# Performance work log

Measured on AMD Instinct MI355X. Metric: run time of the kernel, lower is better.

## Reference

```python
import jax, jax.numpy as jnp
from jax import lax
import numpy as np

CIN, COUT, K, STYLE_DIM = 256, 256, 3, 512
N_LAYERS = 4
TYPES = ("same", "upsample", "same", "downsample")
SCALE = 1.0 / float(np.sqrt(CIN * K ** 2))  # source uses kernel_size**2 even in 1D
EPS = 1e-8
_BK = np.array([1.0, 3.0, 3.0, 1.0], dtype=np.float32)
BLUR_K = _BK / _BK.sum()  # normalized FIR kernel, len 4


def _blur(x, kern, pad):
    # x: (B, C, L); depthwise FIR correlation after zero-padding (upfirdn1d, up=down=1)
    B, C, _ = x.shape
    xp = jnp.pad(x, ((0, 0), (0, 0), (pad[0], pad[1])))
    w = jnp.broadcast_to(kern.astype(x.dtype)[None, None, :], (C, 1, kern.shape[0]))
    return lax.conv_general_dilated(xp, w, (1,), 'VALID', feature_group_count=C,
                                    dimension_numbers=('NCH', 'OIH', 'NCH'))


def _conv_same(x, w):
    # x: (Cin, L), w: (Cout, Cin, K); padding = (K-1)//2, stride 1
    p = (K - 1) // 2
    return lax.conv_general_dilated(x[None], w, (1,), [(p, p)],
                                    dimension_numbers=('NCH', 'OIH', 'NCH'))[0]


def _conv_down(x, w):
    # stride-2 valid conv (padding handled by preceding blur)
    return lax.conv_general_dilated(x[None], w, (2,), 'VALID',
                                    dimension_numbers=('NCH', 'OIH', 'NCH'))[0]


def _conv_up(x, w_t):
    # torch conv_transpose1d(stride=2, padding=0); w_t: (Cin, Cout, K)
    return lax.conv_transpose(x[None], w_t, (2,), 'VALID',
                              dimension_numbers=('NCH', 'IOH', 'NCH'),
                              transpose_kernel=True)[0]


def _layer(x, style, w, b, mw, mb, typ):
    # style modulation: s = Linear(style) -> (B, Cin)
    s = style @ mw.T + mb
    weight = (SCALE * w) * s[:, None, :, None]              # (B, Cout, Cin, K)
    demod = lax.rsqrt(jnp.sum(weight * weight, axis=(2, 3)) + EPS)
    weight = weight * demod[:, :, None, None]
    blur_k = jnp.asarray(BLUR_K)
    if typ == 'same':
        out = jax.vmap(_conv_same)(x, weight) + b[None, :, None]
    elif typ == 'upsample':
        # bias added by conv_transpose BEFORE blur (kernel_scale=2, pad=(1,1) for k=3, kb=4)
        out = jax.vmap(_conv_up)(x, weight.transpose(0, 2, 1, 3)) + b[None, :, None]
        out = _blur(out, 2.0 * blur_k, (1, 1))
    elif typ == 'downsample':
        # blur first (kernel_scale=1, pad=(2,2) for k=3, kb=4), then stride-2 conv
        xb = _blur(x, blur_k, (2, 2))
        out = jax.vmap(_conv_down)(xb, weight) + b[None, :, None]
    else:
        raise NotImplementedError(typ)
    return out


def setup_inputs() -> dict:
    key = jax.random.key(0)
    ks = jax.random.split(key, 6)
    B, L = 16, 4096
    return {
        'x': jax.random.normal(ks[0], (B, CIN, L), dtype=jnp.float32),
        'style': jax.random.normal(ks[1], (B, STYLE_DIM), dtype=jnp.float32),
        'weights': jax.random.normal(ks[2], (N_LAYERS, COUT, CIN, K), dtype=jnp.float32),
        'biases': jax.random.normal(ks[3], (N_LAYERS, COUT), dtype=jnp.float32) * 0.1,
        'mod_w': jax.random.normal(ks[4], (N_LAYERS, CIN, STYLE_DIM), dtype=jnp.float32) / np.sqrt(STYLE_DIM),
        'mod_b': 1.0 + 0.1 * jax.random.normal(ks[5], (N_LAYERS, CIN), dtype=jnp.float32),
    }


def reference(x, style, weights, biases, mod_w, mod_b):
    out = x
    for i, typ in enumerate(TYPES):
        out = _layer(out, style, weights[i], biases[i], mod_w[i], mod_b[i], typ)
    return out
```

## Files before the change

kernel.cpp:

```cpp
#include <hip/hip_runtime.h>
#include <math.h>
#include <stddef.h>

#define CIN 256
#define COUT 256
#define SD 512
#define NB 16
#define KSCALE (1.0f / 48.0f)
#define MEPS 1e-8f
#define SRROW 8320

typedef __attribute__((ext_vector_type(8))) short short8;
typedef __attribute__((ext_vector_type(4))) float floatx4;
typedef unsigned short ushort;

__device__ inline ushort f2bf(float f) {
    union { float f; unsigned int u; } v; v.f = f;
    unsigned int u = v.u;
    return (ushort)((u + 0x7FFFu + ((u >> 16) & 1u)) >> 16);
}
__device__ inline float bf2f(ushort h) {
    union { unsigned int u; float f; } v; v.u = ((unsigned int)h) << 16;
    return v.f;
}

__device__ inline void gload16(const ushort* g, ushort* l) {
    __builtin_amdgcn_global_load_lds(
        (const __attribute__((address_space(1))) unsigned int*)g,
        (__attribute__((address_space(3))) unsigned int*)l,
        16, 0, 0);
}

__global__ __launch_bounds__(256) void modwprep_k(
    const float* __restrict__ style, const float* __restrict__ weights,
    const float* __restrict__ mod_w, const float* __restrict__ mod_b,
    float* __restrict__ s_all, float* __restrict__ demod_all,
    ushort* __restrict__ Wbf)
{
    int t = threadIdx.x;
    if (blockIdx.x < 64) {
        int layer = blockIdx.x >> 4;
        int b = blockIdx.x & 15;
        __shared__ float st[SD];
        __shared__ float s2[CIN];

        for (int j = t; j < SD; j += 256) st[j] = style[b * SD + j];
        __syncthreads();

        const float* mw = mod_w + ((size_t)layer * CIN + t) * SD;
        float acc = 0.f;
        for (int j = 0; j < SD; ++j) acc += mw[j] * st[j];
        float s = acc + mod_b[layer * CIN + t];
        s_all[((size_t)layer * NB + b) * CIN + t] = s;
        s2[t] = s * s;
        __syncthreads();

        const float* wr = weights + ((size_t)layer * COUT + t) * (CIN * 3);
        float d = 0.f;
        for (int ci = 0; ci < CIN; ++ci) {
            float w0 = wr[ci * 3 + 0], w1 = wr[ci * 3 + 1], w2 = wr[ci * 3 + 2];
            d += (w0 * w0 + w1 * w1 + w2 * w2) * s2[ci];
        }
        demod_all[((size_t)layer * NB + b) * CIN + t] = rsqrtf(KSCALE * KSCALE * d + MEPS);
    } else {
        int lin = blockIdx.x - 64;
        int layer = lin >> 8;
        int idx = (lin & 255) * 256 + t;
        int a = idx >> 8, c = idx & 255;
        ushort* wl = Wbf + (size_t)layer * 196608;
        if (layer == 1) {
            const float* src = weights + ((size_t)1 * 196608) + ((size_t)c * 256 + a) * 3;
            #pragma unroll
            for (int k = 0; k < 3; ++k)
                wl[(size_t)k * 65536 + a * 256 + c] = f2bf(src[k]);
        } else {
            const float* src = weights + ((size_t)layer * 196608) + ((size_t)a * 256 + c) * 3;
            #pragma unroll
            for (int k = 0; k < 3; ++k)
                wl[(size_t)a * 768 + k * 256 + c] = f2bf(src[k]);
        }
    }
}

__global__ __launch_bounds__(256) void xprep_k(
    const float* __restrict__ x, const float* __restrict__ s0,
    ushort* __restrict__ Tout)
{
    __shared__ ushort lt[64 * 72];
    int l0 = blockIdx.x * 64, ci0 = blockIdx.y * 64;
    int b = blockIdx.z;
    int t = threadIdx.x;
    const float* xb = x + (size_t)b * CIN * 4096;
    const float* sb = s0 + b * CIN;

    for (int idx = t; idx < 64 * 64; idx += 256) {
        int ci = idx >> 6, lc = idx & 63;
        float v = xb[(size_t)(ci0 + ci) * 4096 + l0 + lc] * sb[ci0 + ci];
        lt[lc * 72 + ci] = f2bf(v);
    }
    __syncthreads();
    ushort* ob = Tout + (size_t)b * SRROW * 256;
    for (int idx = t; idx < 64 * 8; idx += 256) {
        int lc = idx >> 3, ch = idx & 7;
        short8 v = *(const short8*)&lt[lc * 72 + ch * 8];
        *(short8*)&ob[(size_t)(l0 + lc) * 256 + ci0 + ch * 8] = v;
    }
    if (blockIdx.x == 0 && t < 64)
        *(ob - 256 + ci0 + t) = 0;
    if (blockIdx.x == 63 && t < 128) {
        int r = 4096 + (t >> 6);
        ob[(size_t)r * 256 + ci0 + (t & 63)] = 0;
    }
}

__global__ __launch_bounds__(256) void blur_bf16_k(
    const ushort* __restrict__ in, int Lin,
    ushort* __restrict__ outp, int Lout,
    const float* __restrict__ scale,
    int pad, float c0, float c1, float c2, float c3,
    int gfront, int gback)
{
    int b = blockIdx.y;
    int idx = blockIdx.x * 256 + threadIdx.x;
    if (idx >= (gfront + Lout + gback) * 32) return;
    int row = (idx >> 5) - gfront;
    int ci = (idx & 31) * 8;
    ushort* ob = outp + (size_t)b * SRROW * 256;
    if (row < 0 || row >= Lout) {
        short8 z = {0, 0, 0, 0, 0, 0, 0, 0};
        *(short8*)(ob + (ptrdiff_t)row * 256 + ci) = z;
        return;
    }
    const ushort* ib = in + (size_t)b * SRROW * 256;
    float acc[8] = {};
    int base = row - pad;
    float cf[4] = {c0, c1, c2, c3};
    #pragma unroll
    for (int i = 0; i < 4; ++i) {
        int r = base + i;
        if (r >= 0 && r < Lin) {
            short8 v = *(const short8*)&ib[(size_t)r * 256 + ci];
            #pragma unroll
            for (int j = 0; j < 8; ++j) acc[j] += cf[i] * bf2f((ushort)v[j]);
        }
    }
    short8 o;
    #pragma unroll
    for (int j = 0; j < 8; ++j) {
        float sv = scale[b * CIN + ci + j];
        o[j] = (short)f2bf(acc[j] * sv);
    }
    *(short8*)&ob[(size_t)row * 256 + ci] = o;
}

__global__ __launch_bounds__(512, 4) void conv_same_mfma(
    const ushort* __restrict__ Tin, int Lmax,
    const ushort* __restrict__ Wl,
    const float* __restrict__ dm, const float* __restrict__ post, float postScale,
    const float* __restrict__ bias,
    ushort* __restrict__ Tout, int guardL)
{
    __shared__ __align__(16) ushort S[29184];
    ushort* Xs = S;
    ushort* Ws = S + 16896;
    int l0 = blockIdx.x * 256;
    int cot = blockIdx.y * 64;
    int b = blockIdx.z;
    int t = threadIdx.x;
    int lane = t & 63, wv = t >> 6;
    int lr = lane & 15, lg = lane >> 4;
    int lrow = lane >> 3, cg = lane & 7;

    const ushort* Tb = Tin + (size_t)b * SRROW * 256;

    floatx4 acc[4][2];
    #pragma unroll
    for (int i = 0; i < 4; ++i) { acc[i][0] = (floatx4)0.f; acc[i][1] = (floatx4)0.f; }

    for (int ci0 = 0; ci0 < 256; ci0 += 64) {
        __syncthreads();
        for (int i = wv; i < 24; i += 8) {
            int wr = i * 8 + lrow;
            int co = wr & 63, tap = wr >> 6;
            gload16(Wl + (size_t)(cot + co) * 768 + tap * 256 + ci0 + ((cg ^ (co & 7)) * 8),
                    Ws + i * 512);
        }
        for (int i = wv; i < 33; i += 8) {
            int row = i * 8 + lrow;
            int dr = l0 - 1 + row;
            if (dr > Lmax) dr = Lmax;
            gload16(Tb + (ptrdiff_t)dr * 256 + ci0 + ((cg ^ (row & 7)) * 8),
                    Xs + i * 512);
        }
        __syncthreads();
        #pragma unroll
        for (int tap = 0; tap < 3; ++tap)
            #pragma unroll
            for (int kk = 0; kk < 2; ++kk) {
                short8 a[4];
                #pragma unroll
                for (int mf = 0; mf < 4; ++mf)
                    a[mf] = *(const short8*)&Ws[(tap * 64 + mf * 16 + lr) * 64 + ((kk * 32 + lg * 8) ^ ((lr & 7) * 8))];
                short8 bf[2];
                #pragma unroll
                for (int nf = 0; nf < 2; ++nf) {
                    int row = wv * 32 + nf * 16 + lr + tap;
                    bf[nf] = *(const short8*)&Xs[row * 64 + ((kk * 32 + lg * 8) ^ ((row & 7) * 8))];
                }
                #pragma unroll
                for (int mf = 0; mf < 4; ++mf)
                    #pragma unroll
                    for (int nf = 0; nf < 2; ++nf)
                        acc[mf][nf] = __builtin_amdgcn_mfma_f32_16x16x32_bf16(a[mf], bf[nf], acc[mf][nf], 0, 0, 0);
            }
    }

    __syncthreads();
    ushort* Ot = S;
    #pragma unroll
    for (int mf = 0; mf < 4; ++mf)
        #pragma unroll
        for (int nf = 0; nf < 2; ++nf)
            #pragma unroll
            for (int rg = 0; rg < 4; ++rg) {
                int lo = wv * 32 + nf * 16 + lr;
                int co = mf * 16 + lg * 4 + rg;
                float dmv = dm[b * COUT + cot + co] * KSCALE;
                float v = acc[mf][nf][rg] * dmv + bias[cot + co];
                if (post) v *= post[b * COUT + cot + co] * postScale;
                Ot[lo * 72 + co] = f2bf(v);
            }
    __syncthreads();
    ushort* ob = Tout + (size_t)b * SRROW * 256;
    for (int idx = t; idx < 256 * 8; idx += 512) {
        int lo = idx >> 3, ch = idx & 7;
        short8 v = *(const short8*)&Ot[lo * 72 + ch * 8];
        *(short8*)&ob[(size_t)(l0 + lo) * 256 + cot + ch * 8] = v;
    }
    if (guardL > 0) {
        if (blockIdx.x == 0 && t < 64)
            *(ob - 256 + cot + t) = 0;
        if (l0 + 256 == guardL && t < 128) {
            int r = guardL + (t >> 6);
            ob[(size_t)r * 256 + cot + (t & 63)] = 0;
        }
    }
}

__global__ __launch_bounds__(512, 4) void upconv_mfma(
    const ushort* __restrict__ Tin, int Lout,
    const ushort* __restrict__ Wl,
    const float* __restrict__ s, const float* __restrict__ bias,
    ushort* __restrict__ Tout)
{
    __shared__ __align__(16) ushort S[29184];
    ushort* Xs = S;
    ushort* Ws = S + 16896;
    int m0 = blockIdx.x * 256;
    int ot = blockIdx.y * 64;
    int b = blockIdx.z;
    int t = threadIdx.x;
    int lane = t & 63, wv = t >> 6;
    int lr = lane & 15, lg = lane >> 4;
    int lrow = lane >> 3, cg = lane & 7;

    const ushort* Tb = Tin + (size_t)b * SRROW * 256;

    floatx4 aE[4][2], aO[4][2];
    #pragma unroll
    for (int i = 0; i < 4; ++i)
        #pragma unroll
        for (int j = 0; j < 2; ++j) { aE[i][j] = (floatx4)0.f; aO[i][j] = (floatx4)0.f; }

    for (int ci0 = 0; ci0 < 256; ci0 += 64) {
        __syncthreads();
        for (int i = wv; i < 24; i += 8) {
            int wr = i * 8 + lrow;
            int o = wr & 63, tap = wr >> 6;
            gload16(Wl + (size_t)tap * 65536 + (size_t)(ot + o) * 256 + ci0 + ((cg ^ (o & 7)) * 8),
                    Ws + i * 512);
        }
        for (int i = wv; i < 33; i += 8) {
            int row = i * 8 + lrow;
            gload16(Tb + (ptrdiff_t)(m0 - 1 + row) * 256 + ci0 + ((cg ^ (row & 7)) * 8),
                    Xs + i * 512);
        }
        __syncthreads();
        #pragma unroll
        for (int kk = 0; kk < 2; ++kk) {
            short8 bm1[2], bm[2];
            #pragma unroll
            for (int nf = 0; nf < 2; ++nf) {
                int r0 = wv * 32 + nf * 16 + lr;
                int ci = kk * 32 + lg * 8;
                bm1[nf] = *(const short8*)&Xs[r0 * 64 + (ci ^ ((r0 & 7) * 8))];
                int r1 = r0 + 1;
                bm[nf]  = *(const short8*)&Xs[r1 * 64 + (ci ^ ((r1 & 7) * 8))];
            }
            #pragma unroll
            for (int tap = 0; tap < 3; ++tap) {
                short8 a[4];
                #pragma unroll
                for (int mf = 0; mf < 4; ++mf)
                    a[mf] = *(const short8*)&Ws[(tap * 64 + mf * 16 + lr) * 64 + ((kk * 32 + lg * 8) ^ ((lr & 7) * 8))];
                #pragma unroll
                for (int mf = 0; mf < 4; ++mf)
                    #pragma unroll
                    for (int nf = 0; nf < 2; ++nf) {
                        if (tap == 0) aE[mf][nf] = __builtin_amdgcn_mfma_f32_16x16x32_bf16(a[mf], bm[nf],  aE[mf][nf], 0, 0, 0);
                        if (tap == 2) aE[mf][nf] = __builtin_amdgcn_mfma_f32_16x16x32_bf16(a[mf], bm1[nf], aE[mf][nf], 0, 0, 0);
                        if (tap == 1) aO[mf][nf] = __builtin_amdgcn_mfma_f32_16x16x32_bf16(a[mf], bm[nf],  aO[mf][nf], 0, 0, 0);
                    }
            }
        }
    }

    ushort* Ot = S;
    ushort* ob = Tout + (size_t)b * SRROW * 256;
    __syncthreads();
    if (wv < 4) {
        #pragma unroll
        for (int mf = 0; mf < 4; ++mf)
            #pragma unroll
            for (int nf = 0; nf < 2; ++nf)
                #pragma unroll
                for (int rg = 0; rg < 4; ++rg) {
                    int mloc = wv * 32 + nf * 16 + lr;
                    int co = mf * 16 + lg * 4 + rg;
                    float sv = s[b * COUT + ot + co];
                    float bi = bias[ot + co];
                    Ot[(2 * mloc) * 72 + co]     = f2bf(aE[mf][nf][rg] * sv + bi);
                    Ot[(2 * mloc + 1) * 72 + co] = f2bf(aO[mf][nf][rg] * sv + bi);
                }
    }
    __syncthreads();
    for (int idx = t; idx < 256 * 8; idx += 512) {
        int lo = idx >> 3, ch = idx & 7;
        int n = 2 * m0 + lo;
        if (n < Lout) {
            short8 v = *(const short8*)&Ot[lo * 72 + ch * 8];
            *(short8*)&ob[(size_t)n * 256 + ot + ch * 8] = v;
        }
    }
    __syncthreads();
    if (wv >= 4) {
        #pragma unroll
        for (int mf = 0; mf < 4; ++mf)
            #pragma unroll
            for (int nf = 0; nf < 2; ++nf)
                #pragma unroll
                for (int rg = 0; rg < 4; ++rg) {
                    int mloc = wv * 32 + nf * 16 + lr;
                    int co = mf * 16 + lg * 4 + rg;
                    float sv = s[b * COUT + ot + co];
                    float bi = bias[ot + co];
                    Ot[(2 * mloc - 256) * 72 + co] = f2bf(aE[mf][nf][rg] * sv + bi);
                    Ot[(2 * mloc - 255) * 72 + co] = f2bf(aO[mf][nf][rg] * sv + bi);
                }
    }
    __syncthreads();
    for (int idx = t; idx < 256 * 8; idx += 512) {
        int lo = idx >> 3, ch = idx & 7;
        int n = 2 * m0 + 256 + lo;
        if (n < Lout) {
            short8 v = *(const short8*)&Ot[lo * 72 + ch * 8];
            *(short8*)&ob[(size_t)n * 256 + ot + ch * 8] = v;
        }
    }
}

__global__ __launch_bounds__(512, 4) void conv_down_mfma(
    const ushort* __restrict__ Tin,
    const ushort* __restrict__ Wl,
    const float* __restrict__ dm, const float* __restrict__ bias,
    float* __restrict__ outp)
{
    __shared__ __align__(16) ushort S[29184];
    ushort* Xs = S;
    ushort* Ws = S + 16896;
    int l0 = blockIdx.x * 128;
    int cot = blockIdx.y * 64;
    int b = blockIdx.z;
    int t = threadIdx.x;
    int lane = t & 63, wv = t >> 6;
    int lr = lane & 15, lg = lane >> 4;
    int lrow = lane >> 3, cg = lane & 7;

    const ushort* Tb = Tin + (size_t)b * SRROW * 256;

    floatx4 acc[4];
    #pragma unroll
    for (int i = 0; i < 4; ++i) acc[i] = (floatx4)0.f;

    for (int ci0 = 0; ci0 < 256; ci0 += 64) {
        __syncthreads();
        for (int i = wv; i < 24; i += 8) {
            int wr = i * 8 + lrow;
            int co = wr & 63, tap = wr >> 6;
            gload16(Wl + (size_t)(cot + co) * 768 + tap * 256 + ci0 + ((cg ^ (co & 7)) * 8),
                    Ws + i * 512);
        }
        for (int i = wv; i < 33; i += 8) {
            int row = i * 8 + lrow;
            gload16(Tb + (ptrdiff_t)(2 * l0 + row) * 256 + ci0 + ((cg ^ (row & 7)) * 8),
                    Xs + i * 512);
        }
        __syncthreads();
        #pragma unroll
        for (int tap = 0; tap < 3; ++tap)
            #pragma unroll
            for (int kk = 0; kk < 2; ++kk) {
                short8 a[4];
                #pragma unroll
                for (int mf = 0; mf < 4; ++mf)
                    a[mf] = *(const short8*)&Ws[(tap * 64 + mf * 16 + lr) * 64 + ((kk * 32 + lg * 8) ^ ((lr & 7) * 8))];
                int row = 2 * (wv * 16 + lr) + tap;
                short8 bf = *(const short8*)&Xs[row * 64 + ((kk * 32 + lg * 8) ^ ((row & 7) * 8))];
                #pragma unroll
                for (int mf = 0; mf < 4; ++mf)
                    acc[mf] = __builtin_amdgcn_mfma_f32_16x16x32_bf16(a[mf], bf, acc[mf], 0, 0, 0);
            }
    }

    float* ob = outp + (size_t)b * COUT * 4096;
    #pragma unroll
    for (int mf = 0; mf < 4; ++mf)
        #pragma unroll
        for (int rg = 0; rg < 4; ++rg) {
            int co = cot + mf * 16 + lg * 4 + rg;
            int l = l0 + wv * 16 + lr;
            float dmv = dm[b * COUT + co] * KSCALE;
            ob[(size_t)co * 4096 + l] = acc[mf][rg] * dmv + bias[co];
        }
}

extern "C" void kernel_launch(void* const* d_in, const int* in_sizes, int n_in,
                              void* d_out, int out_size, void* d_ws, size_t ws_size,
                              hipStream_t stream) {
    const float* x       = (const float*)d_in[0];
    const float* style   = (const float*)d_in[1];
    const float* weights = (const float*)d_in[2];
    const float* biases  = (const float*)d_in[3];
    const float* mod_w   = (const float*)d_in[4];
    const float* mod_b   = (const float*)d_in[5];
    float* out = (float*)d_out;

    float* s_all = (float*)d_ws;
    float* demod_all = s_all + 4 * NB * CIN;
    const size_t WBF_OFF = 131072;
    const size_t BUF_OFF = WBF_OFF + 1572864;
    ushort* Wbf = (ushort*)((char*)d_ws + WBF_OFF);
    ushort* bufBase = (ushort*)((char*)d_ws + BUF_OFF);

    const int SL = NB * CIN;
    const size_t perSampleB = (size_t)2 * SRROW * 256 * sizeof(ushort);
    size_t availB = ws_size > BUF_OFF ? ws_size - BUF_OFF : 0;
    int g = (int)(availB / perSampleB);
    if (g < 1) g = 1;
    if (g > NB) g = NB;

    const size_t sElems = (size_t)SRROW * 256;
    ushort* bufAU = bufBase;
    ushort* bufBU = bufBase + (size_t)g * sElems;
    ushort* bufA = bufAU + 512;
    ushort* bufB = bufBU + 512;

    modwprep_k<<<1088, 256, 0, stream>>>(style, weights, mod_w, mod_b,
                                         s_all, demod_all, Wbf);

    for (int b0 = 0; b0 < NB; b0 += g) {
        int gb = NB - b0 < g ? NB - b0 : g;

        xprep_k<<<dim3(64, 4, gb), 256, 0, stream>>>(
            x + (size_t)b0 * CIN * 4096, s_all + 0 * SL + b0 * CIN, bufA);

        conv_same_mfma<<<dim3(16, 4, gb), 512, 0, stream>>>(
            bufA, 4097, Wbf + 0,
            demod_all + 0 * SL + b0 * CIN, demod_all + 1 * SL + b0 * CIN, KSCALE,
            biases + 0 * COUT, bufB, 4096);

        upconv_mfma<<<dim3(17, 4, gb), 512, 0, stream>>>(
            bufB, 8193, Wbf + 196608,
            s_all + 1 * SL + b0 * CIN, biases + 1 * COUT, bufA);

        blur_bf16_k<<<dim3(1025, gb), 256, 0, stream>>>(
            bufA, 8193, bufB, 8192, s_all + 2 * SL + b0 * CIN,
            1, 0.25f, 0.75f, 0.75f, 0.25f, 1, 2);

        conv_same_mfma<<<dim3(32, 4, gb), 512, 0, stream>>>(
            bufB, 8193, Wbf + 393216,
            demod_all + 2 * SL + b0 * CIN, (const float*)nullptr, 1.0f,
            biases + 2 * COUT, bufA, -1);

        blur_bf16_k<<<dim3(1025, gb), 256, 0, stream>>>(
            bufA, 8192, bufB, 8193, s_all + 3 * SL + b0 * CIN,
            2, 0.125f, 0.375f, 0.375f, 0.125f, 0, 0);

        conv_down_mfma<<<dim3(32, 4, gb), 512, 0, stream>>>(
            bufB, Wbf + 589824,
            demod_all + 3 * SL + b0 * CIN, biases + 3 * COUT,
            out + (size_t)b0 * COUT * 4096);
    }
}
```

Measured before the change: 297.7 us.

## Widen conv output-channel tile to 128 and halve the input-channel chunk to 32

```diff
diff --git a/kernel.cpp b/kernel.cpp
--- a/kernel.cpp
+++ b/kernel.cpp
@@ -160,89 +160,98 @@
     const float* __restrict__ bias,
     ushort* __restrict__ Tout, int guardL)
 {
-    __shared__ __align__(16) ushort S[29184];
+    __shared__ __align__(16) ushort S[20992];
     ushort* Xs = S;
-    ushort* Ws = S + 16896;
+    ushort* Ws = S + 8704;
     int l0 = blockIdx.x * 256;
-    int cot = blockIdx.y * 64;
+    int cot = blockIdx.y * 128;
     int b = blockIdx.z;
     int t = threadIdx.x;
     int lane = t & 63, wv = t >> 6;
     int lr = lane & 15, lg = lane >> 4;
-    int lrow = lane >> 3, cg = lane & 7;
+    int srow = lane >> 2, sslot = lane & 3;
 
     const ushort* Tb = Tin + (size_t)b * SRROW * 256;
 
-    floatx4 acc[4][2];
-    #pragma unroll
-    for (int i = 0; i < 4; ++i) { acc[i][0] = (floatx4)0.f; acc[i][1] = (floatx4)0.f; }
-
-    for (int ci0 = 0; ci0 < 256; ci0 += 64) {
-        __syncthreads();
-        for (int i = wv; i < 24; i += 8) {
-            int wr = i * 8 + lrow;
-            int co = wr & 63, tap = wr >> 6;
-            gload16(Wl + (size_t)(cot + co) * 768 + tap * 256 + ci0 + ((cg ^ (co & 7)) * 8),
-                    Ws + i * 512);
-        }
-        for (int i = wv; i < 33; i += 8) {
-            int row = i * 8 + lrow;
-            int dr = l0 - 1 + row;
-            if (dr > Lmax) dr = Lmax;
-            gload16(Tb + (ptrdiff_t)dr * 256 + ci0 + ((cg ^ (row & 7)) * 8),
-                    Xs + i * 512);
-        }
-        __syncthreads();
-        #pragma unroll
-        for (int tap = 0; tap < 3; ++tap)
-            #pragma unroll
-            for (int kk = 0; kk < 2; ++kk) {
+    floatx4 acc[8][2];
+    #pragma unroll
+    for (int i = 0; i < 8; ++i) { acc[i][0] = (floatx4)0.f; acc[i][1] = (floatx4)0.f; }
+
+    for (int ci0 = 0; ci0 < 256; ci0 += 32) {
+        __syncthreads();
+        for (int i = wv; i < 41; i += 8) {
+            if (i < 17) {
+                int ldr = i * 16 + srow;
+                int dr = l0 - 1 + ldr;
+                if (dr > Lmax) dr = Lmax;
+                gload16(Tb + (ptrdiff_t)dr * 256 + ci0 + ((sslot ^ ((ldr >> 1) & 3)) * 8),
+                        Xs + i * 512);
+            } else {
+                int wr = (i - 17) * 16 + srow;
+                int co = wr & 127, tap = wr >> 7;
+                gload16(Wl + (size_t)(cot + co) * 768 + tap * 256 + ci0 + ((sslot ^ ((wr >> 1) & 3)) * 8),
+                        Ws + (i - 17) * 512);
+            }
+        }
+        __syncthreads();
+        #pragma unroll
+        for (int tap = 0; tap < 3; ++tap) {
+            short8 bf[2];
+            #pragma unroll
+            for (int nf = 0; nf < 2; ++nf) {
+                int row = wv * 32 + nf * 16 + lr + tap;
+                bf[nf] = *(const short8*)&Xs[row * 32 + ((lg ^ ((row >> 1) & 3)) * 8)];
+            }
+            #pragma unroll
+            for (int mh = 0; mh < 2; ++mh) {
                 short8 a[4];
                 #pragma unroll
-                for (int mf = 0; mf < 4; ++mf)
-                    a[mf] = *(const short8*)&Ws[(tap * 64 + mf * 16 + lr) * 64 + ((kk * 32 + lg * 8) ^ ((lr & 7) * 8))];
-                short8 bf[2];
-                #pragma unroll
-                for (int nf = 0; nf < 2; ++nf) {
-                    int row = wv * 32 + nf * 16 + lr + tap;
-                    bf[nf] = *(const short8*)&Xs[row * 64 + ((kk * 32 + lg * 8) ^ ((row & 7) * 8))];
+                for (int mf = 0; mf < 4; ++mf) {
+                    int wr = tap * 128 + (mh * 4 + mf) * 16 + lr;
+                    a[mf] = *(const short8*)&Ws[wr * 32 + ((lg ^ ((wr >> 1) & 3)) * 8)];
                 }
                 #pragma unroll
                 for (int mf = 0; mf < 4; ++mf)
                     #pragma unroll
                     for (int nf = 0; nf < 2; ++nf)
-                        acc[mf][nf] = __builtin_amdgcn_mfma_f32_16x16x32_bf16(a[mf], bf[nf], acc[mf][nf], 0, 0, 0);
-            }
-    }
-
-    __syncthreads();
+                        acc[mh * 4 + mf][nf] =
+                            __builtin_amdgcn_mfma_f32_16x16x32_bf16(a[mf], bf[nf], acc[mh * 4 + mf][nf], 0, 0, 0);
+            }
+        }
+    }
+
     ushort* Ot = S;
-    #pragma unroll
-    for (int mf = 0; mf < 4; ++mf)
-        #pragma unroll
-        for (int nf = 0; nf < 2; ++nf)
-            #pragma unroll
-            for (int rg = 0; rg < 4; ++rg) {
-                int lo = wv * 32 + nf * 16 + lr;
-                int co = mf * 16 + lg * 4 + rg;
-                float dmv = dm[b * COUT + cot + co] * KSCALE;
-                float v = acc[mf][nf][rg] * dmv + bias[cot + co];
-                if (post) v *= post[b * COUT + cot + co] * postScale;
-                Ot[lo * 72 + co] = f2bf(v);
-            }
-    __syncthreads();
     ushort* ob = Tout + (size_t)b * SRROW * 256;
-    for (int idx = t; idx < 256 * 8; idx += 512) {
-        int lo = idx >> 3, ch = idx & 7;
-        short8 v = *(const short8*)&Ot[lo * 72 + ch * 8];
-        *(short8*)&ob[(size_t)(l0 + lo) * 256 + cot + ch * 8] = v;
+    #pragma unroll
+    for (int half = 0; half < 2; ++half) {
+        __syncthreads();
+        #pragma unroll
+        for (int mf = 0; mf < 4; ++mf)
+            #pragma unroll
+            for (int nf = 0; nf < 2; ++nf)
+                #pragma unroll
+                for (int rg = 0; rg < 4; ++rg) {
+                    int lo = wv * 32 + nf * 16 + lr;
+                    int col = mf * 16 + lg * 4 + rg;
+                    int co = cot + half * 64 + col;
+                    float dmv = dm[b * COUT + co] * KSCALE;
+                    float v = acc[half * 4 + mf][nf][rg] * dmv + bias[co];
+                    if (post) v *= post[b * COUT + co] * postScale;
+                    Ot[lo * 72 + col] = f2bf(v);
+                }
+        __syncthreads();
+        for (int idx = t; idx < 256 * 8; idx += 512) {
+            int lo = idx >> 3, ch = idx & 7;
+            short8 v = *(const short8*)&Ot[lo * 72 + ch * 8];
+            *(short8*)&ob[(size_t)(l0 + lo) * 256 + cot + half * 64 + ch * 8] = v;
+        }
     }
     if (guardL > 0) {
-        if (blockIdx.x == 0 && t < 64)
+        if (blockIdx.x == 0 && t < 128)
             *(ob - 256 + cot + t) = 0;
-        if (l0 + 256 == guardL && t < 128) {
-            int r = guardL + (t >> 6);
-            ob[(size_t)r * 256 + cot + (t & 63)] = 0;
+        if (l0 + 256 == guardL && t < 256) {
+            int r = guardL + (t >> 7);
+            ob[(size_t)r * 256 + cot + (t & 127)] = 0;
         }
     }
 }
@@ -375,56 +384,61 @@
     const float* __restrict__ dm, const float* __restrict__ bias,
     float* __restrict__ outp)
 {
-    __shared__ __align__(16) ushort S[29184];
+    __shared__ __align__(16) ushort S[20992];
     ushort* Xs = S;
-    ushort* Ws = S + 16896;
+    ushort* Ws = S + 8704;
     int l0 = blockIdx.x * 128;
-    int cot = blockIdx.y * 64;
+    int cot = blockIdx.y * 128;
     int b = blockIdx.z;
     int t = threadIdx.x;
     int lane = t & 63, wv = t >> 6;
     int lr = lane & 15, lg = lane >> 4;
-    int lrow = lane >> 3, cg = lane & 7;
+    int srow = lane >> 2, sslot = lane & 3;
 
     const ushort* Tb = Tin + (size_t)b * SRROW * 256;
 
-    floatx4 acc[4];
-    #pragma unroll
-    for (int i = 0; i < 4; ++i) acc[i] = (floatx4)0.f;
-
-    for (int ci0 = 0; ci0 < 256; ci0 += 64) {
-        __syncthreads();
-        for (int i = wv; i < 24; i += 8) {
-            int wr = i * 8 + lrow;
-            int co = wr & 63, tap = wr >> 6;
-            gload16(Wl + (size_t)(cot + co) * 768 + tap * 256 + ci0 + ((cg ^ (co & 7)) * 8),
-                    Ws + i * 512);
-        }
-        for (int i = wv; i < 33; i += 8) {
-            int row = i * 8 + lrow;
-            gload16(Tb + (ptrdiff_t)(2 * l0 + row) * 256 + ci0 + ((cg ^ (row & 7)) * 8),
-                    Xs + i * 512);
-        }
-        __syncthreads();
-        #pragma unroll
-        for (int tap = 0; tap < 3; ++tap)
-            #pragma unroll
-            for (int kk = 0; kk < 2; ++kk) {
+    floatx4 acc[8];
+    #pragma unroll
+    for (int i = 0; i < 8; ++i) acc[i] = (floatx4)0.f;
+
+    for (int ci0 = 0; ci0 < 256; ci0 += 32) {
+        __syncthreads();
+        for (int i = wv; i < 41; i += 8) {
+            if (i < 17) {
+                int ldr = i * 16 + srow;
+                gload16(Tb + (ptrdiff_t)(2 * l0 + ldr) * 256 + ci0 + ((sslot ^ ((ldr >> 1) & 3)) * 8),
+                        Xs + i * 512);
+            } else {
+                int wr = (i - 17) * 16 + srow;
+                int co = wr & 127, tap = wr >> 7;
+                gload16(Wl + (size_t)(cot + co) * 768 + tap * 256 + ci0 + ((sslot ^ ((wr >> 1) & 3)) * 8),
+                        Ws + (i - 17) * 512);
+            }
+        }
+        __syncthreads();
+        #pragma unroll
+        for (int tap = 0; tap < 3; ++tap) {
+            int row = 2 * (wv * 16 + lr) + tap;
+            short8 bf = *(const short8*)&Xs[row * 32 + ((lg ^ ((row >> 1) & 3)) * 8)];
+            #pragma unroll
+            for (int mh = 0; mh < 2; ++mh) {
                 short8 a[4];
                 #pragma unroll
+                for (int mf = 0; mf < 4; ++mf) {
+                    int wr = tap * 128 + (mh * 4 + mf) * 16 + lr;
+                    a[mf] = *(const short8*)&Ws[wr * 32 + ((lg ^ ((wr >> 1) & 3)) * 8)];
+                }
+                #pragma unroll
                 for (int mf = 0; mf < 4; ++mf)
-                    a[mf] = *(const short8*)&Ws[(tap * 64 + mf * 16 + lr) * 64 + ((kk * 32 + lg * 8) ^ ((lr & 7) * 8))];
-                int row = 2 * (wv * 16 + lr) + tap;
-                short8 bf = *(const short8*)&Xs[row * 64 + ((kk * 32 + lg * 8) ^ ((row & 7) * 8))];
-                #pragma unroll
-                for (int mf = 0; mf < 4; ++mf)
-                    acc[mf] = __builtin_amdgcn_mfma_f32_16x16x32_bf16(a[mf], bf, acc[mf], 0, 0, 0);
-            }
+                    acc[mh * 4 + mf] =
+                        __builtin_amdgcn_mfma_f32_16x16x32_bf16(a[mf], bf, acc[mh * 4 + mf], 0, 0, 0);
+            }
+        }
     }
 
     float* ob = outp + (size_t)b * COUT * 4096;
     #pragma unroll
-    for (int mf = 0; mf < 4; ++mf)
+    for (int mf = 0; mf < 8; ++mf)
         #pragma unroll
         for (int rg = 0; rg < 4; ++rg) {
             int co = cot + mf * 16 + lg * 4 + rg;
@@ -474,7 +488,7 @@
         xprep_k<<<dim3(64, 4, gb), 256, 0, stream>>>(
             x + (size_t)b0 * CIN * 4096, s_all + 0 * SL + b0 * CIN, bufA);
 
-        conv_same_mfma<<<dim3(16, 4, gb), 512, 0, stream>>>(
+        conv_same_mfma<<<dim3(16, 2, gb), 512, 0, stream>>>(
             bufA, 4097, Wbf + 0,
             demod_all + 0 * SL + b0 * CIN, demod_all + 1 * SL + b0 * CIN, KSCALE,
             biases + 0 * COUT, bufB, 4096);
@@ -487,7 +501,7 @@
             bufA, 8193, bufB, 8192, s_all + 2 * SL + b0 * CIN,
             1, 0.25f, 0.75f, 0.75f, 0.25f, 1, 2);
 
-        conv_same_mfma<<<dim3(32, 4, gb), 512, 0, stream>>>(
+        conv_same_mfma<<<dim3(32, 2, gb), 512, 0, stream>>>(
             bufB, 8193, Wbf + 393216,
             demod_all + 2 * SL + b0 * CIN, (const float*)nullptr, 1.0f,
             biases + 2 * COUT, bufA, -1);
@@ -496,7 +510,7 @@
             bufA, 8192, bufB, 8193, s_all + 3 * SL + b0 * CIN,
             2, 0.125f, 0.375f, 0.375f, 0.125f, 0, 0);
 
-        conv_down_mfma<<<dim3(32, 4, gb), 512, 0, stream>>>(
+        conv_down_mfma<<<dim3(32, 2, gb), 512, 0, stream>>>(
             bufB, Wbf + 589824,
             demod_all + 3 * SL + b0 * CIN, biases + 3 * COUT,
             out + (size_t)b0 * COUT * 4096);
```

Result: no change. 302.5 us (+1.6%).
